# Kernel optimization log

Hardware: AMD Instinct MI355X
Metric: run time of the kernel (lower is better)

## Reference

```python
import jax, jax.numpy as jnp
import numpy as np
from jax import lax

V, H, B, S, NSLOT, T, G, NSW = 20000, 400, 16, 256, 30, 10, 3, 40


def setup_inputs() -> dict:
    key = jax.random.key(0)
    ks = jax.random.split(key, 24)
    p = lambda k, shape: jax.random.normal(k, shape, dtype=jnp.float32) * 0.1
    return {
        'story': jax.random.randint(ks[0], (B, S), 0, V),
        'enc_lens': jax.random.randint(ks[1], (B,), S // 2, S + 1),
        'target_batches': jax.random.randint(ks[2], (B, NSLOT, T), 0, V),
        'domain_idx': jax.random.randint(ks[3], (NSLOT,), 0, NSW),
        'slot_idx': jax.random.randint(ks[4], (NSLOT,), 0, NSW),
        'emb': p(ks[5], (V, H)),
        'enc_Wih_f': p(ks[6], (3 * H, H)), 'enc_Whh_f': p(ks[7], (3 * H, H)),
        'enc_bih_f': p(ks[8], (3 * H,)), 'enc_bhh_f': p(ks[9], (3 * H,)),
        'enc_Wih_b': p(ks[10], (3 * H, H)), 'enc_Whh_b': p(ks[11], (3 * H, H)),
        'enc_bih_b': p(ks[12], (3 * H,)), 'enc_bhh_b': p(ks[13], (3 * H,)),
        'dec_Wih': p(ks[14], (3 * H, H)), 'dec_Whh': p(ks[15], (3 * H, H)),
        'dec_bih': p(ks[16], (3 * H,)), 'dec_bhh': p(ks[17], (3 * H,)),
        'Wr': p(ks[18], (1, 3 * H)), 'br': p(ks[19], (1,)),
        'Wg': p(ks[20], (G, H)), 'bg': p(ks[21], (G,)),
        'slot_table': p(ks[22], (NSW, H)),
    }


def _gru_scan(x, m, h0, Wih, Whh, bih, bhh):
    # x: [S,B,H], m: [S,B] validity mask (packed-sequence semantics)
    def step(h, xm):
        xt, mt = xm
        gi = xt @ Wih.T + bih
        gh = h @ Whh.T + bhh
        ir, iz, inn = jnp.split(gi, 3, -1)
        hr, hz, hn = jnp.split(gh, 3, -1)
        r = jax.nn.sigmoid(ir + hr)
        z = jax.nn.sigmoid(iz + hz)
        n = jnp.tanh(inn + r * hn)
        hnew = (1.0 - z) * n + z * h
        h = jnp.where(mt[:, None], hnew, h)
        y = jnp.where(mt[:, None], hnew, 0.0)
        return h, y
    hT, ys = lax.scan(step, h0, (x, m))
    return ys, hT


def reference(story, enc_lens, target_batches, domain_idx, slot_idx, emb,
              enc_Wih_f, enc_Whh_f, enc_bih_f, enc_bhh_f,
              enc_Wih_b, enc_Whh_b, enc_bih_b, enc_bhh_b,
              dec_Wih, dec_Whh, dec_bih, dec_bhh,
              Wr, br, Wg, bg, slot_table):
    Bc, Sc = story.shape
    nslot = domain_idx.shape[0]
    Tc = target_batches.shape[2]
    NB = nslot * Bc

    # ----- EncoderRNN: bidirectional GRU over story (seq-major) -----
    x = emb[story.T]                                   # [S,B,H]
    mask = jnp.arange(Sc)[:, None] < enc_lens[None, :]  # [S,B]
    h0 = jnp.zeros((Bc, H), jnp.float32)
    ys_f, h_f = _gru_scan(x, mask, h0, enc_Wih_f, enc_Whh_f, enc_bih_f, enc_bhh_f)
    ys_b, h_b = _gru_scan(x[::-1], mask[::-1], h0, enc_Wih_b, enc_Whh_b, enc_bih_b, enc_bhh_b)
    ys_b = ys_b[::-1]
    encoded_outputs = (ys_f + ys_b).transpose(1, 0, 2)  # [B,S,H]
    enc_hidden = h_f + h_b                              # [B,H]

    # ----- Generator (parallel decode, teacher forcing) -----
    combined = slot_table[domain_idx] + slot_table[slot_idx]           # [nslot,H]
    slot_emb_arr = jnp.repeat(combined[:, None, :], Bc, axis=1).reshape(NB, H)
    hidden0 = jnp.tile(enc_hidden, (nslot, 1))                         # [NB,H]
    enc_out = jnp.tile(encoded_outputs, (nslot, 1, 1))                 # [NB,S,H]
    lens_rep = jnp.tile(enc_lens, nslot)
    story_rep = jnp.tile(story, (nslot, 1))                            # [NB,S]
    attn_mask = jnp.arange(Sc)[None, :] < lens_rep[:, None]            # [NB,S]
    rows = jnp.arange(NB)[:, None]

    # teacher-forced decoder inputs: step0 = slot emb, then gold tokens
    tgt_flat = target_batches.transpose(1, 0, 2).reshape(NB, Tc)       # [NB,T]
    dec_in = jnp.concatenate([slot_emb_arr[None], emb[tgt_flat[:, :Tc - 1].T]], axis=0)  # [T,NB,H]

    def dec_step(h, x_in):
        gi = x_in @ dec_Wih.T + dec_bih
        gh = h @ dec_Whh.T + dec_bhh
        ir, iz, inn = jnp.split(gi, 3, -1)
        hr, hz, hn = jnp.split(gh, 3, -1)
        r = jax.nn.sigmoid(ir + hr)
        z = jax.nn.sigmoid(iz + hz)
        n = jnp.tanh(inn + r * hn)
        h = (1.0 - z) * n + z * h                      # dec_state == new hidden
        scores = jnp.einsum('nh,nsh->ns', h, enc_out)
        scores = jnp.where(attn_mask, scores, -jnp.inf)
        prob = jax.nn.softmax(scores, axis=1)          # [NB,S]
        context = jnp.einsum('ns,nsh->nh', prob, enc_out)
        p_vocab = jax.nn.softmax(h @ emb.T, axis=1)    # [NB,V]
        p_gen_vec = jnp.concatenate([h, context, x_in], axis=-1)
        sw = jax.nn.sigmoid(p_gen_vec @ Wr.T + br)     # [NB,1]
        p_ctx = jnp.zeros_like(p_vocab).at[rows, story_rep].add(prob)
        final_p = (1.0 - sw) * p_ctx + sw * p_vocab
        return h, (final_p, context)

    _, (finals, contexts) = lax.scan(dec_step, hidden0, dec_in)
    all_point_outputs = finals.reshape(Tc, nslot, Bc, V).transpose(1, 2, 0, 3)  # [nslot,B,T,V]
    all_gate_outputs = (contexts[0] @ Wg.T + bg).reshape(nslot, Bc, G)
    return all_point_outputs, all_gate_outputs
```

## Files before the change

kernel.cpp:

```cpp
#include <hip/hip_runtime.h>
#include <hip/hip_bf16.h>

typedef unsigned short u16;
typedef __attribute__((ext_vector_type(8))) short bf16x8;
typedef __attribute__((ext_vector_type(4))) float f32x4;
typedef __attribute__((ext_vector_type(4))) unsigned u32x4;

static constexpr int V = 20000, H = 400, B = 16, S = 256, NSLOT = 30, T = 10, G = 3;
static constexpr int H3 = 3 * H;
static constexpr int NB = NSLOT * B;
static constexpr int MM = T * NB;
static constexpr int ENBLK = 20;
static constexpr int ESL   = 20;
static constexpr int EROWS = 64;
static constexpr int EKP   = 416;
static constexpr int ENC_BLOCKS = 2 * ENBLK;
static constexpr int DGI_TM = (MM + 63) / 64;
static constexpr int DGI_TN = (H3 + 63) / 64;
static constexpr int DGI_TILES = DGI_TM * DGI_TN;
static constexpr int HP2 = 424;
static constexpr int SCP = 260;
static constexpr int PP  = 264;
static constexpr int CXP = 404;
static constexpr int FUSED_LDS = 32*HP2*2 + 32*SCP*4 + 32*PP*2 + 32*CXP*4;
static constexpr int NE = V * H;
static constexpr int NW = H3 * H;
static constexpr int NP = 2 * ENBLK * EROWS * EKP;

__device__ __forceinline__ float bf2f(u16 v) {
    union { unsigned u; float f; } x; x.u = ((unsigned)v) << 16; return x.f;
}
__device__ __forceinline__ u16 f2bf(float f) {
    union { float f; unsigned u; } x; x.f = f;
    unsigned r = x.u + 0x7fffu + ((x.u >> 16) & 1u);
    return (u16)(r >> 16);
}
__device__ __forceinline__ float sigm(float v) { return 1.f / (1.f + __expf(-v)); }

__global__ __launch_bounds__(256) void gemm_bt(
    const u16* __restrict__ A, const u16* __restrict__ Bt,
    const float* __restrict__ bias, float* __restrict__ C,
    int M, int N, int K, int lda, int ldb, long long ldc)
{
    __shared__ u16 As[64][40];
    __shared__ u16 Bs[64][40];
    const int m0 = blockIdx.x * 64, n0 = blockIdx.y * 64;
    const int tid = threadIdx.x, wave = tid >> 6, lane = tid & 63;
    const int wm = (wave >> 1) * 32, wn = (wave & 1) * 32;
    const int srow = tid >> 2, scol = (tid & 3) * 8;
    const int fr = lane & 15, kq = lane >> 4;
    f32x4 acc[2][2];
#pragma unroll
    for (int i = 0; i < 2; ++i)
#pragma unroll
        for (int j = 0; j < 2; ++j) acc[i][j] = (f32x4){0.f, 0.f, 0.f, 0.f};

    for (int k0 = 0; k0 < K; k0 += 32) {
        {
            int gr = m0 + srow, gc = k0 + scol;
            bf16x8 v;
            if (gr < M && gc + 8 <= K) {
                v = *(const bf16x8*)(A + (long long)gr * lda + gc);
            } else {
                short tmp[8];
#pragma unroll
                for (int j = 0; j < 8; ++j)
                    tmp[j] = (gr < M && gc + j < K) ? (short)A[(long long)gr * lda + gc + j] : (short)0;
                v = *(bf16x8*)tmp;
            }
            *(bf16x8*)&As[srow][scol] = v;
        }
        {
            int gr = n0 + srow, gc = k0 + scol;
            bf16x8 v;
            if (gr < N && gc + 8 <= K) {
                v = *(const bf16x8*)(Bt + (long long)gr * ldb + gc);
            } else {
                short tmp[8];
#pragma unroll
                for (int j = 0; j < 8; ++j)
                    tmp[j] = (gr < N && gc + j < K) ? (short)Bt[(long long)gr * ldb + gc + j] : (short)0;
                v = *(bf16x8*)tmp;
            }
            *(bf16x8*)&Bs[srow][scol] = v;
        }
        __syncthreads();
        bf16x8 af[2], bfr[2];
#pragma unroll
        for (int i = 0; i < 2; ++i) af[i]  = *(const bf16x8*)&As[wm + i * 16 + fr][kq * 8];
#pragma unroll
        for (int j = 0; j < 2; ++j) bfr[j] = *(const bf16x8*)&Bs[wn + j * 16 + fr][kq * 8];
#pragma unroll
        for (int i = 0; i < 2; ++i)
#pragma unroll
            for (int j = 0; j < 2; ++j)
                acc[i][j] = __builtin_amdgcn_mfma_f32_16x16x32_bf16(af[i], bfr[j], acc[i][j], 0, 0, 0);
        __syncthreads();
    }

#pragma unroll
    for (int i = 0; i < 2; ++i)
#pragma unroll
        for (int j = 0; j < 2; ++j) {
            int col = n0 + wn + j * 16 + fr;
            float bv = (bias != nullptr && col < N) ? bias[col] : 0.f;
#pragma unroll
            for (int r = 0; r < 4; ++r) {
                int row = m0 + wm + i * 16 + kq * 4 + r;
                if (row < M && col < N) C[(long long)row * ldc + col] = acc[i][j][r] + bv;
            }
        }
}

__global__ __launch_bounds__(256) void gemm_xw2_kernel(
    const u16* __restrict__ A,
    const u16* __restrict__ W0, const u16* __restrict__ W1,
    const float* __restrict__ b0, const float* __restrict__ b1,
    float* __restrict__ C0, float* __restrict__ C1)
{
    const int z = blockIdx.z;
    const u16* Bt = z ? W1 : W0;
    const float* bias = z ? b1 : b0;
    float* C = z ? C1 : C0;
    const int M = S * B, N = H3, K = H;

    __shared__ u16 As[64][40];
    __shared__ u16 Bs[64][40];
    const int m0 = blockIdx.x * 64, n0 = blockIdx.y * 64;
    const int tid = threadIdx.x, wave = tid >> 6, lane = tid & 63;
    const int wm = (wave >> 1) * 32, wn = (wave & 1) * 32;
    const int srow = tid >> 2, scol = (tid & 3) * 8;
    const int fr = lane & 15, kq = lane >> 4;
    f32x4 acc[2][2];
#pragma unroll
    for (int i = 0; i < 2; ++i)
#pragma unroll
        for (int j = 0; j < 2; ++j) acc[i][j] = (f32x4){0.f, 0.f, 0.f, 0.f};

    for (int k0 = 0; k0 < K; k0 += 32) {
        {
            int gr = m0 + srow, gc = k0 + scol;
            bf16x8 v = (bf16x8){0,0,0,0,0,0,0,0};
            if (gr < M && gc + 8 <= K) v = *(const bf16x8*)(A + (long long)gr * K + gc);
            *(bf16x8*)&As[srow][scol] = v;
        }
        {
            int gr = n0 + srow, gc = k0 + scol;
            bf16x8 v = (bf16x8){0,0,0,0,0,0,0,0};
            if (gr < N && gc + 8 <= K) v = *(const bf16x8*)(Bt + (long long)gr * K + gc);
            *(bf16x8*)&Bs[srow][scol] = v;
        }
        __syncthreads();
        bf16x8 af[2], bfr[2];
#pragma unroll
        for (int i = 0; i < 2; ++i) af[i]  = *(const bf16x8*)&As[wm + i * 16 + fr][kq * 8];
#pragma unroll
        for (int j = 0; j < 2; ++j) bfr[j] = *(const bf16x8*)&Bs[wn + j * 16 + fr][kq * 8];
#pragma unroll
        for (int i = 0; i < 2; ++i)
#pragma unroll
            for (int j = 0; j < 2; ++j)
                acc[i][j] = __builtin_amdgcn_mfma_f32_16x16x32_bf16(af[i], bfr[j], acc[i][j], 0, 0, 0);
        __syncthreads();
    }

#pragma unroll
    for (int i = 0; i < 2; ++i)
#pragma unroll
        for (int j = 0; j < 2; ++j) {
            int col = n0 + wn + j * 16 + fr;
            float bv = (col < N) ? bias[col] : 0.f;
#pragma unroll
            for (int r = 0; r < 4; ++r) {
                int row = m0 + wm + i * 16 + kq * 4 + r;
                if (row < M && col < N) C[(long long)row * H3 + col] = acc[i][j][r] + bv;
            }
        }
}

__global__ __launch_bounds__(256) void vocab_gemm_kernel(
    const u16* __restrict__ A, const u16* __restrict__ Bt,
    float* __restrict__ C, float* __restrict__ rowsum)
{
    __shared__ u16 As[128][40];
    __shared__ u16 Bs[128][40];
    const int m0 = blockIdx.x * 128, n0 = blockIdx.y * 128;
    const int tid = threadIdx.x, wave = tid >> 6, lane = tid & 63;
    const int wm = (wave >> 1) * 64, wn = (wave & 1) * 64;
    const int srow = tid >> 1, scol = (tid & 1) * 16;
    const int fr = lane & 15, kq = lane >> 4;
    f32x4 acc[4][4];
#pragma unroll
    for (int i = 0; i < 4; ++i)
#pragma unroll
        for (int j = 0; j < 4; ++j) acc[i][j] = (f32x4){0.f, 0.f, 0.f, 0.f};

    for (int k0 = 0; k0 < H; k0 += 32) {
        {
            int gr = m0 + srow, gc = k0 + scol;
            bf16x8 v0 = (bf16x8){0,0,0,0,0,0,0,0}, v1 = v0;
            if (gr < MM) {
                const u16* src = A + (long long)gr * H + gc;
                if (gc + 8 <= H)  v0 = *(const bf16x8*)src;
                if (gc + 16 <= H) v1 = *(const bf16x8*)(src + 8);
            }
            *(bf16x8*)&As[srow][scol] = v0;
            *(bf16x8*)&As[srow][scol + 8] = v1;
        }
        {
            int gr = n0 + srow, gc = k0 + scol;
            bf16x8 v0 = (bf16x8){0,0,0,0,0,0,0,0}, v1 = v0;
            if (gr < V) {
                const u16* src = Bt + (long long)gr * H + gc;
                if (gc + 8 <= H)  v0 = *(const bf16x8*)src;
                if (gc + 16 <= H) v1 = *(const bf16x8*)(src + 8);
            }
            *(bf16x8*)&Bs[srow][scol] = v0;
            *(bf16x8*)&Bs[srow][scol + 8] = v1;
        }
        __syncthreads();
        bf16x8 af[4], bfr[4];
#pragma unroll
        for (int i = 0; i < 4; ++i) af[i]  = *(const bf16x8*)&As[wm + i * 16 + fr][kq * 8];
#pragma unroll
        for (int j = 0; j < 4; ++j) bfr[j] = *(const bf16x8*)&Bs[wn + j * 16 + fr][kq * 8];
#pragma unroll
        for (int i = 0; i < 4; ++i)
#pragma unroll
            for (int j = 0; j < 4; ++j)
                acc[i][j] = __builtin_amdgcn_mfma_f32_16x16x32_bf16(af[i], bfr[j], acc[i][j], 0, 0, 0);
        __syncthreads();
    }

#pragma unroll
    for (int i = 0; i < 4; ++i)
#pragma unroll
        for (int j = 0; j < 4; ++j)
#pragma unroll
            for (int r = 0; r < 4; ++r) {
                int row = m0 + wm + i * 16 + kq * 4 + r;
                int col = n0 + wn + j * 16 + fr;
                bool ok = (row < MM) && (col < V);
                float v = ok ? __expf(acc[i][j][r]) : 0.f;
                acc[i][j][r] = v;
                if (ok) {
                    int n = row % NB, t = row / NB;
                    C[((long long)n * T + t) * V + col] = v;
                }
            }
#pragma unroll
    for (int i = 0; i < 4; ++i)
#pragma unroll
        for (int r = 0; r < 4; ++r) {
            float s = acc[i][0][r] + acc[i][1][r] + acc[i][2][r] + acc[i][3][r];
            s += __shfl_xor(s, 1); s += __shfl_xor(s, 2);
            s += __shfl_xor(s, 4); s += __shfl_xor(s, 8);
            if (fr == 0) {
                int row = m0 + wm + i * 16 + kq * 4 + r;
                if (row < MM) atomicAdd(&rowsum[row], s);
            }
        }
}

__global__ void prep_all_kernel(
    const float* __restrict__ emb, u16* __restrict__ embb,
    const float* __restrict__ wihf, u16* __restrict__ wihfb,
    const float* __restrict__ wihb, u16* __restrict__ wihbb,
    const float* __restrict__ dwih, u16* __restrict__ dwihb,
    const float* __restrict__ dwhh, u16* __restrict__ dwhhb,
    const float* __restrict__ whhf, const float* __restrict__ whhb,
    u16* __restrict__ wencp)
{
    const int total = NE + 4 * NW + NP;
    for (int i = blockIdx.x * blockDim.x + threadIdx.x; i < total;
         i += gridDim.x * blockDim.x) {
        if (i < NE) { embb[i] = f2bf(emb[i]); continue; }
        int i2 = i - NE;
        if (i2 < NW) { wihfb[i2] = f2bf(wihf[i2]); continue; }
        i2 -= NW;
        if (i2 < NW) { wihbb[i2] = f2bf(wihb[i2]); continue; }
        i2 -= NW;
        if (i2 < NW) { dwihb[i2] = f2bf(dwih[i2]); continue; }
        i2 -= NW;
        if (i2 < NW) { dwhhb[i2] = f2bf(dwhh[i2]); continue; }
        i2 -= NW;
        int k = i2 % EKP; int r = i2 / EKP;
        int rloc = r % EROWS; r /= EROWS;
        int j = r % ENBLK; int dir = r / ENBLK;
        u16 v = 0;
        if (k < H && rloc < 3 * ESL) {
            int g = rloc / ESL, c = rloc % ESL;
            const float* W = dir ? whhb : whhf;
            v = f2bf(W[(long long)(g * H + j * ESL + c) * H + k]);
        }
        wencp[i2] = v;
    }
}

__global__ void embed_decin_kernel(
    const int* __restrict__ story, const u16* __restrict__ embb,
    u16* __restrict__ xb,
    const int* __restrict__ tgt, const int* __restrict__ dom,
    const int* __restrict__ sidx, const float* __restrict__ slt,
    u16* __restrict__ decin)
{
    int row = blockIdx.x;
    if (row < S * B) {
        int s = row >> 4, b = row & 15;
        int tok = story[b * S + s];
        const u16* e = embb + (long long)tok * H;
        u16* d = xb + (long long)row * H;
        for (int k = threadIdx.x; k < H; k += blockDim.x) d[k] = e[k];
    } else {
        int i = row - S * B;
        int t = i / NB, n = i % NB;
        int b = n & 15, slot = n >> 4;
        u16* d = decin + ((long long)t * NB + n) * H;
        if (t == 0) {
            const float* s1 = slt + (long long)dom[slot] * H;
            const float* s2 = slt + (long long)sidx[slot] * H;
            for (int k = threadIdx.x; k < H; k += blockDim.x) d[k] = f2bf(s1[k] + s2[k]);
        } else {
            int tok = tgt[(b * NSLOT + slot) * T + (t - 1)];
            const u16* e = embb + (long long)tok * H;
            for (int k = threadIdx.x; k < H; k += blockDim.x) d[k] = e[k];
        }
    }
}

__global__ __launch_bounds__(256) void enc_dgi_kernel(
    const u16* __restrict__ wencp,
    const float* __restrict__ bhhf, const float* __restrict__ bhhb,
    const float* __restrict__ gif, const float* __restrict__ gib,
    const int* __restrict__ lens,
    unsigned* __restrict__ hbuf, int* __restrict__ flags,
    float* __restrict__ ysf, float* __restrict__ ysb,
    float* __restrict__ hfo, float* __restrict__ hbo,
    const u16* __restrict__ decinb, const u16* __restrict__ dwhib,
    const float* __restrict__ dbih, float* __restrict__ dgi)
{
    __shared__ __align__(16) char ldsu[EROWS * EKP * 2 + EROWS * 17 * 4];
    const int tid = threadIdx.x, wave = tid >> 6, lane = tid & 63;
// ... 100 lines not shown

        f32x4 acc = (f32x4){0.f, 0.f, 0.f, 0.f};
        if (t > 0) {
            const int* fl = flg_d + (t - 1) * ENBLK;
            for (;;) {
                int v = 1;
                if (lane < ENBLK)
                    v = __hip_atomic_load(&fl[lane], __ATOMIC_RELAXED,
                                          __HIP_MEMORY_SCOPE_AGENT);
                if (__all(v != 0)) break;
                __builtin_amdgcn_s_sleep(2);
            }
            asm volatile("" ::: "memory");
            const unsigned* hrow = hb_d + ((long long)(t - 1) * B + fr) * EKP + kq * 8;
            f32x4 acch = (f32x4){0.f, 0.f, 0.f, 0.f};
            f32x4 accl = (f32x4){0.f, 0.f, 0.f, 0.f};
#pragma unroll
            for (int kk = 0; kk < 13; ++kk) {
                u32x4 a = *(const u32x4*)(hrow + kk * 32);
                u32x4 b = *(const u32x4*)(hrow + kk * 32 + 4);
                union { unsigned u[4]; bf16x8 v; } hi, lo;
                hi.u[0] = __builtin_amdgcn_perm(a[1], a[0], 0x05040100u);
                hi.u[1] = __builtin_amdgcn_perm(a[3], a[2], 0x05040100u);
                hi.u[2] = __builtin_amdgcn_perm(b[1], b[0], 0x05040100u);
                hi.u[3] = __builtin_amdgcn_perm(b[3], b[2], 0x05040100u);
                lo.u[0] = __builtin_amdgcn_perm(a[1], a[0], 0x07060302u);
                lo.u[1] = __builtin_amdgcn_perm(a[3], a[2], 0x07060302u);
                lo.u[2] = __builtin_amdgcn_perm(b[1], b[0], 0x07060302u);
                lo.u[3] = __builtin_amdgcn_perm(b[3], b[2], 0x07060302u);
                bf16x8 av = *(const bf16x8*)(arow + kk * 32);
                acch = __builtin_amdgcn_mfma_f32_16x16x32_bf16(av, hi.v, acch, 0, 0, 0);
                accl = __builtin_amdgcn_mfma_f32_16x16x32_bf16(av, lo.v, accl, 0, 0, 0);
            }
            acc = acch + accl;
        }
#pragma unroll
        for (int r = 0; r < 4; ++r) ghs[(wave * 16 + kq * 4 + r) * 17 + fr] = acc[r];
        __syncthreads();

        unsigned* hpub = hb_d + (long long)t * B * EKP;
        {
            float ghr = ghs[kl0 * 17 + b0];
            float ghz = ghs[(ESL + kl0) * 17 + b0];
            float ghn = ghs[(2 * ESL + kl0) * 17 + b0];
            float rg = sigm(gr0 + ghr + bhr0);
            float zg = sigm(gz0 + ghz + bhz0);
            float ng = tanhf(gn0 + rg * (ghn + bhn0));
            float hn = (1.f - zg) * ng + zg * h0r;
            bool msk = s < len0;
            float y = msk ? hn : 0.f;
            if (msk) h0r = hn;
            ys[((long long)(b0 * S + s)) * H + k0 + kl0] = y;
            u16 hi = f2bf(h0r);
            unsigned packed = (unsigned)hi | ((unsigned)f2bf(h0r - bf2f(hi)) << 16);
            __hip_atomic_store(&hpub[b0 * EKP + k0 + kl0], packed, __ATOMIC_RELAXED,
                               __HIP_MEMORY_SCOPE_AGENT);
        }
        if (has1) {
            float ghr = ghs[kl1 * 17 + b1];
            float ghz = ghs[(ESL + kl1) * 17 + b1];
            float ghn = ghs[(2 * ESL + kl1) * 17 + b1];
            float rg = sigm(gr1 + ghr + bhr1);
            float zg = sigm(gz1 + ghz + bhz1);
            float ng = tanhf(gn1 + rg * (ghn + bhn1));
            float hn = (1.f - zg) * ng + zg * h1r;
            bool msk = s < len1;
            float y = msk ? hn : 0.f;
            if (msk) h1r = hn;
            ys[((long long)(b1 * S + s)) * H + k0 + kl1] = y;
            u16 hi = f2bf(h1r);
            unsigned packed = (unsigned)hi | ((unsigned)f2bf(h1r - bf2f(hi)) << 16);
            __hip_atomic_store(&hpub[b1 * EKP + k0 + kl1], packed, __ATOMIC_RELAXED,
                               __HIP_MEMORY_SCOPE_AGENT);
        }
        __syncthreads();
        if (tid == 0)
            __hip_atomic_store(&flg_d[t * ENBLK + j], 1, __ATOMIC_RELAXED,
                               __HIP_MEMORY_SCOPE_AGENT);
    }
    ho[b0 * H + k0 + kl0] = h0r;
    if (has1) ho[b1 * H + k0 + kl1] = h1r;
}

__global__ void packE_kernel(const float* __restrict__ ysf, const float* __restrict__ ysb,
                             u16* __restrict__ E, u16* __restrict__ ET) {
    __shared__ u16 tile[32][400];
    const int b = blockIdx.x, s0 = blockIdx.y * 32;
    for (int si = 0; si < 32; ++si) {
        const long long base = ((long long)b * S + s0 + si) * H;
        for (int k = threadIdx.x; k < H; k += blockDim.x) {
            u16 v = f2bf(ysf[base + k] + ysb[base + k]);
            E[base + k] = v;
            tile[si][k] = v;
        }
    }
    __syncthreads();
    for (int idx = threadIdx.x; idx < 32 * H; idx += blockDim.x) {
        int k = idx >> 5, si = idx & 31;
        ET[((long long)b * H + k) * S + s0 + si] = tile[si][k];
    }
}

__global__ void h0_kernel(const float* __restrict__ hf, const float* __restrict__ hb,
                          float* __restrict__ hf32, u16* __restrict__ hnk) {
    int n = blockIdx.x, b = n & 15;
    for (int k = threadIdx.x; k < H; k += blockDim.x) {
        float v = hf[b * H + k] + hb[b * H + k];
        hf32[(long long)n * H + k] = v;
        hnk[(long long)n * H + k] = f2bf(v);
    }
}

__global__ __launch_bounds__(512) void fused_step_kernel(
    const float* __restrict__ dgi, const float* __restrict__ dgh,
    float* __restrict__ hf32, u16* __restrict__ hall,
    const u16* __restrict__ decinb,
    const u16* __restrict__ Eb, const u16* __restrict__ ETb,
    const int* __restrict__ lens,
    const float* __restrict__ Wr, const float* __restrict__ br,
    const float* __restrict__ Wg, const float* __restrict__ bg,
    float* __restrict__ probfT, float* __restrict__ swvT,
    float* __restrict__ gout, int t)
{
    extern __shared__ char smem[];
    u16*   hls = (u16*)smem;
    float* scs = (float*)(smem + 32 * HP2 * 2);
    u16*   pls = (u16*)(smem + 32 * HP2 * 2 + 32 * SCP * 4);
    float* cxs = (float*)(smem + 32 * HP2 * 2 + 32 * SCP * 4 + 32 * PP * 2);

    const int b = blockIdx.x;
    const int tid = threadIdx.x, wave = tid >> 6, lane = tid & 63;
    const int fr = lane & 15, kq = lane >> 4;
    const int len = lens[b];

    for (int i = tid; i < 32 * (HP2 - H); i += 512) {
        int r = i / (HP2 - H), c = H + i % (HP2 - H);
        hls[r * HP2 + c] = 0;
    }
    for (int i = tid; i < 2 * HP2; i += 512) hls[30 * HP2 + i] = 0;
    for (int i = tid; i < 2 * PP; i += 512) pls[30 * PP + i] = 0;

    for (int i = tid; i < 30 * H; i += 512) {
        int slot = i / H, k = i % H;
        int n = slot * 16 + b;
        const float* gi = dgi + ((long long)t * NB + n) * H3;
        const float* gh = dgh + (long long)n * H3;
        float r  = sigm(gi[k] + gh[k]);
        float z  = sigm(gi[H + k] + gh[H + k]);
        float nn = tanhf(gi[2 * H + k] + r * gh[2 * H + k]);
        float h  = hf32[(long long)n * H + k];
        float hn = (1.f - z) * nn + z * h;
        hf32[(long long)n * H + k] = hn;
        u16 hb = f2bf(hn);
        hall[((long long)t * NB + n) * H + k] = hb;
        hls[slot * HP2 + k] = hb;
    }
    __syncthreads();

    {
        const int nt0 = wave * 2;
        f32x4 acc[2][2];
#pragma unroll
        for (int i = 0; i < 2; ++i)
#pragma unroll
            for (int jj = 0; jj < 2; ++jj) acc[i][jj] = (f32x4){0.f, 0.f, 0.f, 0.f};
        const u16* br0 = Eb + ((long long)b * S + nt0 * 16 + fr) * H + kq * 8;
        const u16* br1 = Eb + ((long long)b * S + (nt0 + 1) * 16 + fr) * H + kq * 8;
        const u16* ar0 = hls + fr * HP2 + kq * 8;
        const u16* ar1 = hls + (16 + fr) * HP2 + kq * 8;
#pragma unroll
        for (int kk = 0; kk < 13; ++kk) {
            bf16x8 av0 = *(const bf16x8*)(ar0 + kk * 32);
            bf16x8 av1 = *(const bf16x8*)(ar1 + kk * 32);
            bf16x8 bv0, bv1;
            if (kk == 12 && kq >= 2) {
                bv0 = (bf16x8){0,0,0,0,0,0,0,0}; bv1 = bv0;
            } else {
                bv0 = *(const bf16x8*)(br0 + kk * 32);
                bv1 = *(const bf16x8*)(br1 + kk * 32);
            }
            acc[0][0] = __builtin_amdgcn_mfma_f32_16x16x32_bf16(av0, bv0, acc[0][0], 0, 0, 0);
            acc[1][0] = __builtin_amdgcn_mfma_f32_16x16x32_bf16(av1, bv0, acc[1][0], 0, 0, 0);
            acc[0][1] = __builtin_amdgcn_mfma_f32_16x16x32_bf16(av0, bv1, acc[0][1], 0, 0, 0);
            acc[1][1] = __builtin_amdgcn_mfma_f32_16x16x32_bf16(av1, bv1, acc[1][1], 0, 0, 0);
        }
#pragma unroll
        for (int i = 0; i < 2; ++i)
#pragma unroll
            for (int jj = 0; jj < 2; ++jj)
#pragma unroll
                for (int r = 0; r < 4; ++r)
                    scs[(i * 16 + kq * 4 + r) * SCP + (nt0 + jj) * 16 + fr] = acc[i][jj][r];
    }
    __syncthreads();

    for (int i = 0; i < 4; ++i) {
        int row = wave * 4 + i;
        if (row >= 30) break;
        int n = row * 16 + b;
        float v[4];
        float mx = -3.0e38f;
#pragma unroll
        for (int q = 0; q < 4; ++q) {
            int s = lane + 64 * q;
            float x = (s < len) ? scs[row * SCP + s] : -3.0e38f;
            v[q] = x; mx = fmaxf(mx, x);
        }
        mx = fmaxf(mx, __shfl_xor(mx, 1));  mx = fmaxf(mx, __shfl_xor(mx, 2));
        mx = fmaxf(mx, __shfl_xor(mx, 4));  mx = fmaxf(mx, __shfl_xor(mx, 8));
        mx = fmaxf(mx, __shfl_xor(mx, 16)); mx = fmaxf(mx, __shfl_xor(mx, 32));
        float sum = 0.f;
#pragma unroll
        for (int q = 0; q < 4; ++q) {
            int s = lane + 64 * q;
            float e = (s < len) ? __expf(v[q] - mx) : 0.f;
            v[q] = e; sum += e;
        }
        sum += __shfl_xor(sum, 1);  sum += __shfl_xor(sum, 2);
        sum += __shfl_xor(sum, 4);  sum += __shfl_xor(sum, 8);
        sum += __shfl_xor(sum, 16); sum += __shfl_xor(sum, 32);
        float inv = 1.f / sum;
#pragma unroll
        for (int q = 0; q < 4; ++q) {
            int s = lane + 64 * q;
            float pr = v[q] * inv;
            pls[row * PP + s] = f2bf(pr);
            probfT[((long long)(t * NB + n)) * S + s] = pr;
        }
    }
    __syncthreads();

    for (int nt = wave; nt < 25; nt += 8) {
        f32x4 acc0 = (f32x4){0.f,0.f,0.f,0.f}, acc1 = (f32x4){0.f,0.f,0.f,0.f};
        const u16* brow = ETb + ((long long)b * H + nt * 16 + fr) * S + kq * 8;
        const u16* ar0 = pls + fr * PP + kq * 8;
        const u16* ar1 = pls + (16 + fr) * PP + kq * 8;
#pragma unroll
        for (int kk = 0; kk < 8; ++kk) {
            bf16x8 bv  = *(const bf16x8*)(brow + kk * 32);
            bf16x8 av0 = *(const bf16x8*)(ar0 + kk * 32);
            bf16x8 av1 = *(const bf16x8*)(ar1 + kk * 32);
            acc0 = __builtin_amdgcn_mfma_f32_16x16x32_bf16(av0, bv, acc0, 0, 0, 0);
            acc1 = __builtin_amdgcn_mfma_f32_16x16x32_bf16(av1, bv, acc1, 0, 0, 0);
        }
#pragma unroll
        for (int r = 0; r < 4; ++r) {
            cxs[(kq * 4 + r) * CXP + nt * 16 + fr] = acc0[r];
            cxs[(16 + kq * 4 + r) * CXP + nt * 16 + fr] = acc1[r];
        }
    }
    __syncthreads();

    for (int i = 0; i < 4; ++i) {
        int slot = wave + 8 * i;
        if (slot >= 30) break;
        int n = slot * 16 + b;
        const u16* xrow = decinb + ((long long)t * NB + n) * H;
        float p = 0.f;
        for (int k = lane; k < H; k += 64)
            p += bf2f(hls[slot * HP2 + k]) * Wr[k]
               + cxs[slot * CXP + k] * Wr[H + k]
               + bf2f(xrow[k]) * Wr[2 * H + k];
        p += __shfl_xor(p, 1);  p += __shfl_xor(p, 2);
        p += __shfl_xor(p, 4);  p += __shfl_xor(p, 8);
        p += __shfl_xor(p, 16); p += __shfl_xor(p, 32);
        if (lane == 0) swvT[t * NB + n] = sigm(p + br[0]);
        if (t == 0) {
            for (int g = 0; g < G; ++g) {
                float q = 0.f;
                for (int k = lane; k < H; k += 64)
                    q += cxs[slot * CXP + k] * Wg[g * H + k];
                q += __shfl_xor(q, 1);  q += __shfl_xor(q, 2);
                q += __shfl_xor(q, 4);  q += __shfl_xor(q, 8);
                q += __shfl_xor(q, 16); q += __shfl_xor(q, 32);
                if (lane == 0) gout[(long long)n * G + g] = q + bg[g];
            }
        }
    }
}

__global__ void scale_all_kernel(float* __restrict__ out, const float* __restrict__ swvT,
                                 const float* __restrict__ rowsumT) {
    const int n = blockIdx.x;
    const int col = blockIdx.y * 256 + threadIdx.x;
    if (col >= V) return;
#pragma unroll
    for (int t = 0; t < T; ++t) {
        float f = swvT[t * NB + n] / rowsumT[t * NB + n];
        out[((long long)n * T + t) * V + col] *= f;
    }
}

__global__ void scatter_all_kernel(float* __restrict__ out, const int* __restrict__ story,
                                   const int* __restrict__ lens, const float* __restrict__ swvT,
                                   const float* __restrict__ probfT) {
    const int n = blockIdx.x, t = blockIdx.y, b = n & 15, s = threadIdx.x;
    if (s < lens[b]) {
        int tok = story[b * S + s];
        atomicAdd(out + ((long long)n * T + t) * V + tok,
                  (1.f - swvT[t * NB + n]) * probfT[((long long)(t * NB + n)) * S + s]);
    }
}

extern "C" void kernel_launch(void* const* d_in, const int* in_sizes, int n_in,
                              void* d_out, int out_size, void* d_ws, size_t ws_size,
                              hipStream_t stream) {
    const int*   story = (const int*)d_in[0];
    const int*   lens  = (const int*)d_in[1];
    const int*   tgt   = (const int*)d_in[2];
    const int*   dom   = (const int*)d_in[3];
    const int*   sidx  = (const int*)d_in[4];
    const float* emb   = (const float*)d_in[5];
    const float* wihf  = (const float*)d_in[6];
    const float* whhf  = (const float*)d_in[7];
    const float* bihf  = (const float*)d_in[8];
    const float* bhhf  = (const float*)d_in[9];
    const float* wihb  = (const float*)d_in[10];
    const float* whhb  = (const float*)d_in[11];
    const float* bihb  = (const float*)d_in[12];
    const float* bhhb  = (const float*)d_in[13];
    const float* dwih  = (const float*)d_in[14];
    const float* dwhh  = (const float*)d_in[15];
    const float* dbih  = (const float*)d_in[16];
    const float* dbhh  = (const float*)d_in[17];
    const float* Wr    = (const float*)d_in[18];
    const float* br    = (const float*)d_in[19];
    const float* Wg    = (const float*)d_in[20];
    const float* bg    = (const float*)d_in[21];
    const float* slt   = (const float*)d_in[22];
    float* out = (float*)d_out;

    char* wsb = (char*)d_ws;
    size_t off = 0;
    auto alloc = [&](size_t bytes) -> char* {
        char* p = wsb + off;
        off += (bytes + 255) & ~(size_t)255;
        return p;
    };
    u16*   embb   = (u16*)alloc((size_t)V * H * 2);
    u16*   wihfb  = (u16*)alloc((size_t)H3 * H * 2);
    u16*   wihbb  = (u16*)alloc((size_t)H3 * H * 2);
    u16*   dwihb  = (u16*)alloc((size_t)H3 * H * 2);
    u16*   dwhhb  = (u16*)alloc((size_t)H3 * H * 2);
    u16*   wencp  = (u16*)alloc((size_t)2 * ENBLK * EROWS * EKP * 2);
    unsigned* hbuf = (unsigned*)alloc((size_t)2 * S * B * EKP * 4);
    int*   flags  = (int*)alloc((size_t)2 * S * ENBLK * 4);
    u16*   xb     = (u16*)alloc((size_t)S * B * H * 2);
    u16*   decinb = (u16*)alloc((size_t)T * NB * H * 2);
    float* gif    = (float*)alloc((size_t)S * B * H3 * 4);
    float* gib    = (float*)alloc((size_t)S * B * H3 * 4);
    float* dgi    = (float*)alloc((size_t)T * NB * H3 * 4);
    float* ysf    = (float*)alloc((size_t)B * S * H * 4);
    float* ysb    = (float*)alloc((size_t)B * S * H * 4);
    float* hfv    = (float*)alloc((size_t)B * H * 4);
    float* hbv    = (float*)alloc((size_t)B * H * 4);
    u16*   Eb     = (u16*)alloc((size_t)B * S * H * 2);
    u16*   ETb    = (u16*)alloc((size_t)B * H * S * 2);
    float* hf32   = (float*)alloc((size_t)NB * H * 4);
    u16*   hnk    = (u16*)alloc((size_t)NB * H * 2);
    u16*   hall   = (u16*)alloc((size_t)T * NB * H * 2);
    float* dgh    = (float*)alloc((size_t)NB * H3 * 4);
    float* probfT = (float*)alloc((size_t)T * NB * S * 4);
    float* swvT   = (float*)alloc((size_t)T * NB * 4);
    float* rowsumT = (float*)alloc((size_t)T * NB * 4);
    (void)ws_size; (void)in_sizes; (void)n_in; (void)out_size;

    hipFuncSetAttribute((const void*)fused_step_kernel,
                        hipFuncAttributeMaxDynamicSharedMemorySize, FUSED_LDS);

    hipMemsetAsync(flags, 0, (size_t)2 * S * ENBLK * 4, stream);
    hipMemsetAsync(hbuf, 0, (size_t)2 * S * B * EKP * 4, stream);
    hipMemsetAsync(rowsumT, 0, (size_t)T * NB * 4, stream);
    prep_all_kernel<<<2048, 256, 0, stream>>>(emb, embb, wihf, wihfb, wihb, wihbb,
                                              dwih, dwihb, dwhh, dwhhb,
                                              whhf, whhb, wencp);
    embed_decin_kernel<<<S * B + T * NB, 256, 0, stream>>>(
        story, embb, xb, tgt, dom, sidx, slt, decinb);
    {
        dim3 g((S * B + 63) / 64, (H3 + 63) / 64, 2);
        gemm_xw2_kernel<<<g, 256, 0, stream>>>(xb, wihfb, wihbb, bihf, bihb, gif, gib);
    }

    enc_dgi_kernel<<<ENC_BLOCKS + DGI_TILES, 256, 0, stream>>>(
        wencp, bhhf, bhhb, gif, gib, lens, hbuf, flags, ysf, ysb, hfv, hbv,
        decinb, dwihb, dbih, dgi);
    { dim3 g(B, S / 32); packE_kernel<<<g, 256, 0, stream>>>(ysf, ysb, Eb, ETb); }
    h0_kernel<<<NB, 256, 0, stream>>>(hfv, hbv, hf32, hnk);

    for (int t = 0; t < T; ++t) {
        const u16* hprev = (t == 0) ? hnk : hall + (size_t)(t - 1) * NB * H;
        {
            dim3 g((NB + 63) / 64, (H3 + 63) / 64);
            gemm_bt<<<g, 256, 0, stream>>>(hprev, dwhhb, dbhh, dgh,
                                           NB, H3, H, H, H, H3);
        }
        fused_step_kernel<<<16, 512, FUSED_LDS, stream>>>(
            dgi, dgh, hf32, hall, decinb, Eb, ETb, lens, Wr, br, Wg, bg,
            probfT, swvT, out + (size_t)NB * T * V, t);
    }

    {
        dim3 g((MM + 127) / 128, (V + 127) / 128);
        vocab_gemm_kernel<<<g, 256, 0, stream>>>(hall, embb, out, rowsumT);
    }
    { dim3 g(NB, (V + 255) / 256); scale_all_kernel<<<g, 256, 0, stream>>>(out, swvT, rowsumT); }
    { dim3 g(NB, T); scatter_all_kernel<<<g, 256, 0, stream>>>(out, story, lens, swvT, probfT); }
}
```

Baseline: 2.403 ms.

## Fuse decoder hidden GEMM into step kernel with flag-based intra-grid sync

Merges the per-timestep Whh GEMM and the fused decoder step into one launch. Leading blocks compute dgh tiles and raise per-tile flags, and the 16 step blocks spin on those flags before consuming dgh. This saves ten kernel launches and their inter-kernel gaps. It also merges the packE and h0 kernels into one launch. The risks are deadlock if the consumer blocks get scheduled before the producers and cannot make progress, half-idle 512-thread GEMM blocks, and atomic stores to a per-timestep dgh buffer.

```diff
diff --git a/kernel.cpp b/kernel.cpp
--- a/kernel.cpp
+++ b/kernel.cpp
@@ -18,6 +18,9 @@
 static constexpr int DGI_TM = (MM + 63) / 64;
 static constexpr int DGI_TN = (H3 + 63) / 64;
 static constexpr int DGI_TILES = DGI_TM * DGI_TN;
+static constexpr int DGH_TM = (NB + 63) / 64;
+static constexpr int DGH_TN = (H3 + 63) / 64;
+static constexpr int DGH_TILES = DGH_TM * DGH_TN;
 static constexpr int HP2 = 424;
 static constexpr int SCP = 260;
 static constexpr int PP  = 264;
@@ -36,81 +39,6 @@
     return (u16)(r >> 16);
 }
 __device__ __forceinline__ float sigm(float v) { return 1.f / (1.f + __expf(-v)); }
-
-__global__ __launch_bounds__(256) void gemm_bt(
-    const u16* __restrict__ A, const u16* __restrict__ Bt,
-    const float* __restrict__ bias, float* __restrict__ C,
-    int M, int N, int K, int lda, int ldb, long long ldc)
-{
-    __shared__ u16 As[64][40];
-    __shared__ u16 Bs[64][40];
-    const int m0 = blockIdx.x * 64, n0 = blockIdx.y * 64;
-    const int tid = threadIdx.x, wave = tid >> 6, lane = tid & 63;
-    const int wm = (wave >> 1) * 32, wn = (wave & 1) * 32;
-    const int srow = tid >> 2, scol = (tid & 3) * 8;
-    const int fr = lane & 15, kq = lane >> 4;
-    f32x4 acc[2][2];
-#pragma unroll
-    for (int i = 0; i < 2; ++i)
-#pragma unroll
-        for (int j = 0; j < 2; ++j) acc[i][j] = (f32x4){0.f, 0.f, 0.f, 0.f};
-
-    for (int k0 = 0; k0 < K; k0 += 32) {
-        {
-            int gr = m0 + srow, gc = k0 + scol;
-            bf16x8 v;
-            if (gr < M && gc + 8 <= K) {
-                v = *(const bf16x8*)(A + (long long)gr * lda + gc);
-            } else {
-                short tmp[8];
-#pragma unroll
-                for (int j = 0; j < 8; ++j)
-                    tmp[j] = (gr < M && gc + j < K) ? (short)A[(long long)gr * lda + gc + j] : (short)0;
-                v = *(bf16x8*)tmp;
-            }
-            *(bf16x8*)&As[srow][scol] = v;
-        }
-        {
-            int gr = n0 + srow, gc = k0 + scol;
-            bf16x8 v;
-            if (gr < N && gc + 8 <= K) {
-                v = *(const bf16x8*)(Bt + (long long)gr * ldb + gc);
-            } else {
-                short tmp[8];
-#pragma unroll
-                for (int j = 0; j < 8; ++j)
-                    tmp[j] = (gr < N && gc + j < K) ? (short)Bt[(long long)gr * ldb + gc + j] : (short)0;
-                v = *(bf16x8*)tmp;
-            }
-            *(bf16x8*)&Bs[srow][scol] = v;
-        }
-        __syncthreads();
-        bf16x8 af[2], bfr[2];
-#pragma unroll
-        for (int i = 0; i < 2; ++i) af[i]  = *(const bf16x8*)&As[wm + i * 16 + fr][kq * 8];
-#pragma unroll
-        for (int j = 0; j < 2; ++j) bfr[j] = *(const bf16x8*)&Bs[wn + j * 16 + fr][kq * 8];
-#pragma unroll
-        for (int i = 0; i < 2; ++i)
-#pragma unroll
-            for (int j = 0; j < 2; ++j)
-                acc[i][j] = __builtin_amdgcn_mfma_f32_16x16x32_bf16(af[i], bfr[j], acc[i][j], 0, 0, 0);
-        __syncthreads();
-    }
-
-#pragma unroll
-    for (int i = 0; i < 2; ++i)
-#pragma unroll
-        for (int j = 0; j < 2; ++j) {
-            int col = n0 + wn + j * 16 + fr;
-            float bv = (bias != nullptr && col < N) ? bias[col] : 0.f;
-#pragma unroll
-            for (int r = 0; r < 4; ++r) {
-                int row = m0 + wm + i * 16 + kq * 4 + r;
-                if (row < M && col < N) C[(long long)row * ldc + col] = acc[i][j][r] + bv;
-            }
-        }
-}
 
 __global__ __launch_bounds__(256) void gemm_xw2_kernel(
     const u16* __restrict__ A,
@@ -524,37 +452,44 @@
     if (has1) ho[b1 * H + k0 + kl1] = h1r;
 }
 
-__global__ void packE_kernel(const float* __restrict__ ysf, const float* __restrict__ ysb,
-                             u16* __restrict__ E, u16* __restrict__ ET) {
+__global__ __launch_bounds__(256) void packE_h0_kernel(
+    const float* __restrict__ ysf, const float* __restrict__ ysb,
+    u16* __restrict__ E, u16* __restrict__ ET,
+    const float* __restrict__ hf, const float* __restrict__ hb,
+    float* __restrict__ hf32, u16* __restrict__ hnk)
+{
     __shared__ u16 tile[32][400];
-    const int b = blockIdx.x, s0 = blockIdx.y * 32;
-    for (int si = 0; si < 32; ++si) {
-        const long long base = ((long long)b * S + s0 + si) * H;
+    const int blk = blockIdx.x;
+    if (blk < B * (S / 32)) {
+        const int b = blk / (S / 32), s0 = (blk % (S / 32)) * 32;
+        for (int si = 0; si < 32; ++si) {
+            const long long base = ((long long)b * S + s0 + si) * H;
+            for (int k = threadIdx.x; k < H; k += blockDim.x) {
+                u16 v = f2bf(ysf[base + k] + ysb[base + k]);
+                E[base + k] = v;
+                tile[si][k] = v;
+            }
+        }
+        __syncthreads();
+        for (int idx = threadIdx.x; idx < 32 * H; idx += blockDim.x) {
+            int k = idx >> 5, si = idx & 31;
+            ET[((long long)b * H + k) * S + s0 + si] = tile[si][k];
+        }
+    } else {
+        int n = blk - B * (S / 32), b = n & 15;
         for (int k = threadIdx.x; k < H; k += blockDim.x) {
-            u16 v = f2bf(ysf[base + k] + ysb[base + k]);
-            E[base + k] = v;
-            tile[si][k] = v;
-        }
-    }
-    __syncthreads();
-    for (int idx = threadIdx.x; idx < 32 * H; idx += blockDim.x) {
-        int k = idx >> 5, si = idx & 31;
-        ET[((long long)b * H + k) * S + s0 + si] = tile[si][k];
-    }
-}
-
-__global__ void h0_kernel(const float* __restrict__ hf, const float* __restrict__ hb,
-                          float* __restrict__ hf32, u16* __restrict__ hnk) {
-    int n = blockIdx.x, b = n & 15;
-    for (int k = threadIdx.x; k < H; k += blockDim.x) {
-        float v = hf[b * H + k] + hb[b * H + k];
-        hf32[(long long)n * H + k] = v;
-        hnk[(long long)n * H + k] = f2bf(v);
-    }
-}
-
-__global__ __launch_bounds__(512) void fused_step_kernel(
-    const float* __restrict__ dgi, const float* __restrict__ dgh,
+            float v = hf[b * H + k] + hb[b * H + k];
+            hf32[(long long)n * H + k] = v;
+            hnk[(long long)n * H + k] = f2bf(v);
+        }
+    }
+}
+
+__global__ __launch_bounds__(512) void dec_step_kernel(
+    const u16* __restrict__ hprev, const u16* __restrict__ dwhhb,
+    const float* __restrict__ dbhh,
+    float* __restrict__ dghT, int* __restrict__ dghflg,
+    const float* __restrict__ dgi,
     float* __restrict__ hf32, u16* __restrict__ hall,
     const u16* __restrict__ decinb,
     const u16* __restrict__ Eb, const u16* __restrict__ ETb,
@@ -565,15 +500,85 @@
     float* __restrict__ gout, int t)
 {
     extern __shared__ char smem[];
+    const int tid = threadIdx.x, wave = tid >> 6, lane = tid & 63;
+    const int fr = lane & 15, kq = lane >> 4;
+
+    if (blockIdx.x < DGH_TILES) {
+        u16* As = (u16*)smem;
+        u16* Bs = As + 64 * 40;
+        const int tile = blockIdx.x;
+        const int m0 = (tile % DGH_TM) * 64, n0 = (tile / DGH_TM) * 64;
+        const bool act = (wave < 4);
+        const int wm = (wave >> 1) * 32, wn = (wave & 1) * 32;
+        const int srow = tid >> 2, scol = (tid & 3) * 8;
+        float* C = dghT + (long long)t * NB * H3;
+        f32x4 acc[2][2];
+#pragma unroll
+        for (int i = 0; i < 2; ++i)
+#pragma unroll
+            for (int j = 0; j < 2; ++j) acc[i][j] = (f32x4){0.f, 0.f, 0.f, 0.f};
+
+        for (int k0 = 0; k0 < H; k0 += 32) {
+            if (tid < 256) {
+                {
+                    int gr = m0 + srow, gc = k0 + scol;
+                    bf16x8 v = (bf16x8){0,0,0,0,0,0,0,0};
+                    if (gr < NB && gc + 8 <= H) v = *(const bf16x8*)(hprev + (long long)gr * H + gc);
+                    *(bf16x8*)&As[srow * 40 + scol] = v;
+                }
+                {
+                    int gr = n0 + srow, gc = k0 + scol;
+                    bf16x8 v = (bf16x8){0,0,0,0,0,0,0,0};
+                    if (gr < H3 && gc + 8 <= H) v = *(const bf16x8*)(dwhhb + (long long)gr * H + gc);
+                    *(bf16x8*)&Bs[srow * 40 + scol] = v;
+                }
+            }
+            __syncthreads();
+            if (act) {
+                bf16x8 af[2], bfr[2];
+#pragma unroll
+                for (int i = 0; i < 2; ++i) af[i]  = *(const bf16x8*)&As[(wm + i * 16 + fr) * 40 + kq * 8];
+#pragma unroll
+                for (int j = 0; j < 2; ++j) bfr[j] = *(const bf16x8*)&Bs[(wn + j * 16 + fr) * 40 + kq * 8];
+#pragma unroll
+                for (int i = 0; i < 2; ++i)
+#pragma unroll
+                    for (int j = 0; j < 2; ++j)
+                        acc[i][j] = __builtin_amdgcn_mfma_f32_16x16x32_bf16(af[i], bfr[j], acc[i][j], 0, 0, 0);
+            }
+            __syncthreads();
+        }
+        if (act) {
+#pragma unroll
+            for (int i = 0; i < 2; ++i)
+#pragma unroll
+                for (int j = 0; j < 2; ++j) {
+                    int col = n0 + wn + j * 16 + fr;
+                    float bv = (col < H3) ? dbhh[col] : 0.f;
+#pragma unroll
+                    for (int r = 0; r < 4; ++r) {
+                        int row = m0 + wm + i * 16 + kq * 4 + r;
+                        if (row < NB && col < H3)
+                            __hip_atomic_store(&C[(long long)row * H3 + col], acc[i][j][r] + bv,
+                                               __ATOMIC_RELAXED, __HIP_MEMORY_SCOPE_AGENT);
+                    }
+                }
+        }
+        __syncthreads();
+        if (tid == 0)
+            __hip_atomic_store(&dghflg[t * DGH_TILES + tile], 1, __ATOMIC_RELAXED,
+                               __HIP_MEMORY_SCOPE_AGENT);
+        return;
+    }
+
     u16*   hls = (u16*)smem;
     float* scs = (float*)(smem + 32 * HP2 * 2);
     u16*   pls = (u16*)(smem + 32 * HP2 * 2 + 32 * SCP * 4);
     float* cxs = (float*)(smem + 32 * HP2 * 2 + 32 * SCP * 4 + 32 * PP * 2);
 
-    const int b = blockIdx.x;
-    const int tid = threadIdx.x, wave = tid >> 6, lane = tid & 63;
-    const int fr = lane & 15, kq = lane >> 4;
+    const int b = blockIdx.x - DGH_TILES;
     const int len = lens[b];
+    const float* dgh = dghT + (long long)t * NB * H3;
 
     for (int i = tid; i < 32 * (HP2 - H); i += 512) {
         int r = i / (HP2 - H), c = H + i % (HP2 - H);
@@ -581,6 +586,20 @@
     }
     for (int i = tid; i < 2 * HP2; i += 512) hls[30 * HP2 + i] = 0;
     for (int i = tid; i < 2 * PP; i += 512) pls[30 * PP + i] = 0;
+
+    {
+        const int* fl = dghflg + t * DGH_TILES;
+        for (;;) {
+            int v0 = __hip_atomic_load(&fl[lane], __ATOMIC_RELAXED, __HIP_MEMORY_SCOPE_AGENT);
+            int v1 = (lane + 64 < DGH_TILES)
+                     ? __hip_atomic_load(&fl[lane + 64], __ATOMIC_RELAXED, __HIP_MEMORY_SCOPE_AGENT) : 1;
+            int v2 = (lane + 128 < DGH_TILES)
+                     ? __hip_atomic_load(&fl[lane + 128], __ATOMIC_RELAXED, __HIP_MEMORY_SCOPE_AGENT) : 1;
+            if (__all(v0 != 0 && v1 != 0 && v2 != 0)) break;
+            __builtin_amdgcn_s_sleep(2);
+        }
+        asm volatile("" ::: "memory");
+    }
 
     for (int i = tid; i < 30 * H; i += 512) {
         int slot = i / H, k = i % H;
@@ -801,18 +820,20 @@
     float* hf32   = (float*)alloc((size_t)NB * H * 4);
     u16*   hnk    = (u16*)alloc((size_t)NB * H * 2);
     u16*   hall   = (u16*)alloc((size_t)T * NB * H * 2);
-    float* dgh    = (float*)alloc((size_t)NB * H3 * 4);
+    float* dghT   = (float*)alloc((size_t)T * NB * H3 * 4);
+    int*   dghflg = (int*)alloc((size_t)T * DGH_TILES * 4);
     float* probfT = (float*)alloc((size_t)T * NB * S * 4);
     float* swvT   = (float*)alloc((size_t)T * NB * 4);
     float* rowsumT = (float*)alloc((size_t)T * NB * 4);
     (void)ws_size; (void)in_sizes; (void)n_in; (void)out_size;
 
-    hipFuncSetAttribute((const void*)fused_step_kernel,
+    hipFuncSetAttribute((const void*)dec_step_kernel,
                         hipFuncAttributeMaxDynamicSharedMemorySize, FUSED_LDS);
 
     hipMemsetAsync(flags, 0, (size_t)2 * S * ENBLK * 4, stream);
     hipMemsetAsync(hbuf, 0, (size_t)2 * S * B * EKP * 4, stream);
     hipMemsetAsync(rowsumT, 0, (size_t)T * NB * 4, stream);
+    hipMemsetAsync(dghflg, 0, (size_t)T * DGH_TILES * 4, stream);
     prep_all_kernel<<<2048, 256, 0, stream>>>(emb, embb, wihf, wihfb, wihb, wihbb,
                                               dwih, dwihb, dwhh, dwhhb,
                                               whhf, whhb, wencp);
@@ -826,19 +847,15 @@
     enc_dgi_kernel<<<ENC_BLOCKS + DGI_TILES, 256, 0, stream>>>(
         wencp, bhhf, bhhb, gif, gib, lens, hbuf, flags, ysf, ysb, hfv, hbv,
         decinb, dwihb, dbih, dgi);
-    { dim3 g(B, S / 32); packE_kernel<<<g, 256, 0, stream>>>(ysf, ysb, Eb, ETb); }
-    h0_kernel<<<NB, 256, 0, stream>>>(hfv, hbv, hf32, hnk);
+    packE_h0_kernel<<<B * (S / 32) + NB, 256, 0, stream>>>(
+        ysf, ysb, Eb, ETb, hfv, hbv, hf32, hnk);
 
     for (int t = 0; t < T; ++t) {
         const u16* hprev = (t == 0) ? hnk : hall + (size_t)(t - 1) * NB * H;
-        {
-            dim3 g((NB + 63) / 64, (H3 + 63) / 64);
-            gemm_bt<<<g, 256, 0, stream>>>(hprev, dwhhb, dbhh, dgh,
-                                           NB, H3, H, H, H, H3);
-        }
-        fused_step_kernel<<<16, 512, FUSED_LDS, stream>>>(
-            dgi, dgh, hf32, hall, decinb, Eb, ETb, lens, Wr, br, Wg, bg,
-            probfT, swvT, out + (size_t)NB * T * V, t);
+        dec_step_kernel<<<DGH_TILES + 16, 512, FUSED_LDS, stream>>>(
+            hprev, dwhhb, dbhh, dghT, dghflg, dgi, hf32, hall, decinb,
+            Eb, ETb, lens, Wr, br, Wg, bg, probfT, swvT,
+            out + (size_t)NB * T * V, t);
     }
 
     {
```

New measurement: 2.436 ms. Within noise of the previous version (+1.4%).

## Recompute vocab GEMM in two passes to avoid rescaling the output in memory

Applied to the files above, without the earlier changes.

The vocab softmax now runs as two GEMM passes. The first computes only the exp row sums, and the second recomputes the logits and writes the final scaled probabilities directly. This removes the separate scale kernel, which read and rewrote the whole 192MB output. The cost is doing the 4800x20000x400 GEMM twice. The packE and h0 kernels are also merged into one launch.

```diff
diff --git a/kernel.cpp b/kernel.cpp
--- a/kernel.cpp
+++ b/kernel.cpp
@@ -178,9 +178,9 @@
         }
 }
 
-__global__ __launch_bounds__(256) void vocab_gemm_kernel(
+__global__ __launch_bounds__(256) void vocab_rowsum_kernel(
     const u16* __restrict__ A, const u16* __restrict__ Bt,
-    float* __restrict__ C, float* __restrict__ rowsum)
+    float* __restrict__ rowsum)
 {
     __shared__ u16 As[128][40];
     __shared__ u16 Bs[128][40];
@@ -235,29 +235,89 @@
 #pragma unroll
     for (int i = 0; i < 4; ++i)
 #pragma unroll
-        for (int j = 0; j < 4; ++j)
-#pragma unroll
-            for (int r = 0; r < 4; ++r) {
-                int row = m0 + wm + i * 16 + kq * 4 + r;
+        for (int r = 0; r < 4; ++r) {
+            int row = m0 + wm + i * 16 + kq * 4 + r;
+            float s = 0.f;
+#pragma unroll
+            for (int j = 0; j < 4; ++j) {
                 int col = n0 + wn + j * 16 + fr;
-                bool ok = (row < MM) && (col < V);
-                float v = ok ? __expf(acc[i][j][r]) : 0.f;
-                acc[i][j][r] = v;
-                if (ok) {
-                    int n = row % NB, t = row / NB;
-                    C[((long long)n * T + t) * V + col] = v;
-                }
-            }
-#pragma unroll
-    for (int i = 0; i < 4; ++i)
-#pragma unroll
-        for (int r = 0; r < 4; ++r) {
-            float s = acc[i][0][r] + acc[i][1][r] + acc[i][2][r] + acc[i][3][r];
+                if (row < MM && col < V) s += __expf(acc[i][j][r]);
+            }
             s += __shfl_xor(s, 1); s += __shfl_xor(s, 2);
             s += __shfl_xor(s, 4); s += __shfl_xor(s, 8);
-            if (fr == 0) {
-                int row = m0 + wm + i * 16 + kq * 4 + r;
-                if (row < MM) atomicAdd(&rowsum[row], s);
+            if (fr == 0 && row < MM) atomicAdd(&rowsum[row], s);
+        }
+}
+
+__global__ __launch_bounds__(256) void vocab_write_kernel(
+    const u16* __restrict__ A, const u16* __restrict__ Bt,
+    const float* __restrict__ swvT, const float* __restrict__ rowsum,
+    float* __restrict__ C)
+{
+    __shared__ u16 As[128][40];
+    __shared__ u16 Bs[128][40];
+    const int m0 = blockIdx.x * 128, n0 = blockIdx.y * 128;
+    const int tid = threadIdx.x, wave = tid >> 6, lane = tid & 63;
+    const int wm = (wave >> 1) * 64, wn = (wave & 1) * 64;
+    const int srow = tid >> 1, scol = (tid & 1) * 16;
+    const int fr = lane & 15, kq = lane >> 4;
+    f32x4 acc[4][4];
+#pragma unroll
+    for (int i = 0; i < 4; ++i)
+#pragma unroll
+        for (int j = 0; j < 4; ++j) acc[i][j] = (f32x4){0.f, 0.f, 0.f, 0.f};
+
+    for (int k0 = 0; k0 < H; k0 += 32) {
+        {
+            int gr = m0 + srow, gc = k0 + scol;
+            bf16x8 v0 = (bf16x8){0,0,0,0,0,0,0,0}, v1 = v0;
+            if (gr < MM) {
+                const u16* src = A + (long long)gr * H + gc;
+                if (gc + 8 <= H)  v0 = *(const bf16x8*)src;
+                if (gc + 16 <= H) v1 = *(const bf16x8*)(src + 8);
+            }
+            *(bf16x8*)&As[srow][scol] = v0;
+            *(bf16x8*)&As[srow][scol + 8] = v1;
+        }
+        {
+            int gr = n0 + srow, gc = k0 + scol;
+            bf16x8 v0 = (bf16x8){0,0,0,0,0,0,0,0}, v1 = v0;
+            if (gr < V) {
+                const u16* src = Bt + (long long)gr * H + gc;
+                if (gc + 8 <= H)  v0 = *(const bf16x8*)src;
+                if (gc + 16 <= H) v1 = *(const bf16x8*)(src + 8);
+            }
+            *(bf16x8*)&Bs[srow][scol] = v0;
+            *(bf16x8*)&Bs[srow][scol + 8] = v1;
+        }
+        __syncthreads();
+        bf16x8 af[4], bfr[4];
+#pragma unroll
+        for (int i = 0; i < 4; ++i) af[i]  = *(const bf16x8*)&As[wm + i * 16 + fr][kq * 8];
+#pragma unroll
+        for (int j = 0; j < 4; ++j) bfr[j] = *(const bf16x8*)&Bs[wn + j * 16 + fr][kq * 8];
+#pragma unroll
+        for (int i = 0; i < 4; ++i)
+#pragma unroll
+            for (int j = 0; j < 4; ++j)
+                acc[i][j] = __builtin_amdgcn_mfma_f32_16x16x32_bf16(af[i], bfr[j], acc[i][j], 0, 0, 0);
+        __syncthreads();
+    }
+
+#pragma unroll
+    for (int i = 0; i < 4; ++i)
+#pragma unroll
+        for (int r = 0; r < 4; ++r) {
+            int row = m0 + wm + i * 16 + kq * 4 + r;
+            float f = 0.f;
+            if (row < MM) f = swvT[row] / rowsum[row];
+#pragma unroll
+            for (int j = 0; j < 4; ++j) {
+                int col = n0 + wn + j * 16 + fr;
+                if (row < MM && col < V) {
+                    int n = row % NB, t = row / NB;
+                    C[((long long)n * T + t) * V + col] = __expf(acc[i][j][r]) * f;
+                }
             }
         }
 }
@@ -524,32 +584,36 @@
     if (has1) ho[b1 * H + k0 + kl1] = h1r;
 }
 
-__global__ void packE_kernel(const float* __restrict__ ysf, const float* __restrict__ ysb,
-                             u16* __restrict__ E, u16* __restrict__ ET) {
+__global__ __launch_bounds__(256) void packE_h0_kernel(
+    const float* __restrict__ ysf, const float* __restrict__ ysb,
+    u16* __restrict__ E, u16* __restrict__ ET,
+    const float* __restrict__ hf, const float* __restrict__ hb,
+    float* __restrict__ hf32, u16* __restrict__ hnk)
+{
     __shared__ u16 tile[32][400];
-    const int b = blockIdx.x, s0 = blockIdx.y * 32;
-    for (int si = 0; si < 32; ++si) {
-        const long long base = ((long long)b * S + s0 + si) * H;
+    const int blk = blockIdx.x;
+    if (blk < B * (S / 32)) {
+        const int b = blk / (S / 32), s0 = (blk % (S / 32)) * 32;
+        for (int si = 0; si < 32; ++si) {
+            const long long base = ((long long)b * S + s0 + si) * H;
+            for (int k = threadIdx.x; k < H; k += blockDim.x) {
+                u16 v = f2bf(ysf[base + k] + ysb[base + k]);
+                E[base + k] = v;
+                tile[si][k] = v;
+            }
+        }
+        __syncthreads();
+        for (int idx = threadIdx.x; idx < 32 * H; idx += blockDim.x) {
+            int k = idx >> 5, si = idx & 31;
+            ET[((long long)b * H + k) * S + s0 + si] = tile[si][k];
+        }
+    } else {
+        int n = blk - B * (S / 32), b = n & 15;
         for (int k = threadIdx.x; k < H; k += blockDim.x) {
-            u16 v = f2bf(ysf[base + k] + ysb[base + k]);
-            E[base + k] = v;
-            tile[si][k] = v;
-        }
-    }
-    __syncthreads();
-    for (int idx = threadIdx.x; idx < 32 * H; idx += blockDim.x) {
-        int k = idx >> 5, si = idx & 31;
-        ET[((long long)b * H + k) * S + s0 + si] = tile[si][k];
-    }
-}
-
-__global__ void h0_kernel(const float* __restrict__ hf, const float* __restrict__ hb,
-                          float* __restrict__ hf32, u16* __restrict__ hnk) {
-    int n = blockIdx.x, b = n & 15;
-    for (int k = threadIdx.x; k < H; k += blockDim.x) {
-        float v = hf[b * H + k] + hb[b * H + k];
-        hf32[(long long)n * H + k] = v;
-        hnk[(long long)n * H + k] = f2bf(v);
+            float v = hf[b * H + k] + hb[b * H + k];
+            hf32[(long long)n * H + k] = v;
+            hnk[(long long)n * H + k] = f2bf(v);
+        }
     }
 }
 
@@ -718,18 +782,6 @@
                 if (lane == 0) gout[(long long)n * G + g] = q + bg[g];
             }
         }
-    }
-}
-
-__global__ void scale_all_kernel(float* __restrict__ out, const float* __restrict__ swvT,
-                                 const float* __restrict__ rowsumT) {
-    const int n = blockIdx.x;
-    const int col = blockIdx.y * 256 + threadIdx.x;
-    if (col >= V) return;
-#pragma unroll
-    for (int t = 0; t < T; ++t) {
-        float f = swvT[t * NB + n] / rowsumT[t * NB + n];
-        out[((long long)n * T + t) * V + col] *= f;
     }
 }
 
@@ -826,8 +878,8 @@
     enc_dgi_kernel<<<ENC_BLOCKS + DGI_TILES, 256, 0, stream>>>(
         wencp, bhhf, bhhb, gif, gib, lens, hbuf, flags, ysf, ysb, hfv, hbv,
         decinb, dwihb, dbih, dgi);
-    { dim3 g(B, S / 32); packE_kernel<<<g, 256, 0, stream>>>(ysf, ysb, Eb, ETb); }
-    h0_kernel<<<NB, 256, 0, stream>>>(hfv, hbv, hf32, hnk);
+    packE_h0_kernel<<<B * (S / 32) + NB, 256, 0, stream>>>(
+        ysf, ysb, Eb, ETb, hfv, hbv, hf32, hnk);
 
     for (int t = 0; t < T; ++t) {
         const u16* hprev = (t == 0) ? hnk : hall + (size_t)(t - 1) * NB * H;
@@ -843,8 +895,8 @@
 
     {
         dim3 g((MM + 127) / 128, (V + 127) / 128);
-        vocab_gemm_kernel<<<g, 256, 0, stream>>>(hall, embb, out, rowsumT);
-    }
-    { dim3 g(NB, (V + 255) / 256); scale_all_kernel<<<g, 256, 0, stream>>>(out, swvT, rowsumT); }
+        vocab_rowsum_kernel<<<g, 256, 0, stream>>>(hall, embb, rowsumT);
+        vocab_write_kernel<<<g, 256, 0, stream>>>(hall, embb, swvT, rowsumT, out);
+    }
     { dim3 g(NB, T); scatter_all_kernel<<<g, 256, 0, stream>>>(out, story, lens, swvT, probfT); }
 }
```

Result: faster. 2.306 ms (-4.0%).
